# Performance work log

Measured on AMD Instinct MI355X. Metric: run time of the kernel, lower is better.

## Reference

```python
import jax, jax.numpy as jnp
import numpy as np

HEADS = 16


def fenwick_mask(T):
    # Boolean [T, T] mask: diagonal + Fenwick-tree lookback positions, causal.
    m = np.zeros((T, T), dtype=bool)
    for i in range(T):
        j = i + 1
        while j <= T:
            m[i, j - 1] = True
            j += j & -j
        step = 1
        while i - step >= 0:
            m[i, i - step] = True
            step *= 2
    m &= np.tril(np.ones((T, T), dtype=bool))  # causal
    return jnp.asarray(m)


def setup_inputs() -> dict:
    key = jax.random.key(0)
    ks = jax.random.split(key, 4)
    B, T, C = 2, 2048, 1024
    x = jax.random.normal(ks[0], (B, T, C), dtype=jnp.float32)
    W_qkv = jax.random.normal(ks[1], (C, 3 * C), dtype=jnp.float32) * (C ** -0.5)
    b_qkv = jnp.zeros((3 * C,), dtype=jnp.float32)
    W_proj = jax.random.normal(ks[2], (C, C), dtype=jnp.float32) * (C ** -0.5)
    b_proj = jnp.zeros((C,), dtype=jnp.float32)
    return {"x": x, "W_qkv": W_qkv, "b_qkv": b_qkv, "W_proj": W_proj, "b_proj": b_proj}


def reference(x, W_qkv, b_qkv, W_proj, b_proj):
    B, T, C = x.shape
    H = HEADS
    Dh = C // H
    scale = Dh ** -0.5
    qkv = (x @ W_qkv + b_qkv).reshape(B, T, 3, H, Dh)
    qkv = jnp.transpose(qkv, (2, 0, 3, 1, 4))  # [3, B, H, T, Dh]
    q, k, v = qkv[0], qkv[1], qkv[2]
    attn = jnp.einsum('bhtd,bhsd->bhts', q, k) * scale  # [B, H, T, T]
    mask = fenwick_mask(T)  # trace-time constant
    attn = jnp.where(mask[None, None], attn, -jnp.inf)
    attn = jax.nn.softmax(attn, axis=-1)
    out = jnp.einsum('bhts,bhsd->bhtd', attn, v)  # [B, H, T, Dh]
    out = jnp.transpose(out, (0, 2, 1, 3)).reshape(B, T, C)
    return out @ W_proj + b_proj
```

## Files before the change

kernel.cpp:

```cpp
#include <hip/hip_runtime.h>
#include <hip/hip_bf16.h>


typedef unsigned short ushort_t;
typedef __attribute__((ext_vector_type(8))) short s16x8;
typedef __attribute__((ext_vector_type(4))) float f32x4;

#define T_SEQ 2048
#define C_DIM 1024
#define HEADS 16

__device__ __forceinline__ ushort_t f2bf(float f) {
    union { float f; unsigned u; } v{f};
    unsigned r = v.u + 0x7FFFu + ((v.u >> 16) & 1u);
    return (ushort_t)(r >> 16);
}
__device__ __forceinline__ float bf2f(ushort_t u) {
    union { unsigned u; float f; } v{((unsigned)u) << 16};
    return v.f;
}

__device__ __forceinline__ void async16(const ushort_t* g, ushort_t* l) {
    __builtin_amdgcn_global_load_lds(
        (const __attribute__((address_space(1))) void*)g,
        (__attribute__((address_space(3))) void*)l, 16, 0, 0);
}

__global__ void cvt_bf16(const float* __restrict__ in, ushort_t* __restrict__ out, int n4) {
    int i = blockIdx.x * blockDim.x + threadIdx.x;
    if (i < n4) {
        float4 f = ((const float4*)in)[i];
        ushort4 o;
        o.x = f2bf(f.x); o.y = f2bf(f.y); o.z = f2bf(f.z); o.w = f2bf(f.w);
        ((ushort4*)out)[i] = o;
    }
}

__global__ void transpose_bf16(const float* __restrict__ W, ushort_t* __restrict__ WT,
                               int K, int N) {
    __shared__ ushort_t tile[32][33];
    int nb = blockIdx.x * 32, kb = blockIdx.y * 32;
    int tx = threadIdx.x, ty = threadIdx.y;
    #pragma unroll
    for (int i = ty; i < 32; i += 8)
        tile[i][tx] = f2bf(W[(size_t)(kb + i) * N + nb + tx]);
    __syncthreads();
    #pragma unroll
    for (int i = ty; i < 32; i += 8)
        WT[(size_t)(nb + i) * K + kb + tx] = tile[tx][i];
}

template <bool OUT_BF16>
__global__ void gemm_bt(const ushort_t* __restrict__ A, const ushort_t* __restrict__ BT,
                        const float* __restrict__ bias, void* __restrict__ C,
                        int N, int K) {
    __shared__ ushort_t lsA[128 * 64];
    __shared__ ushort_t lsB[128 * 64];

    const int tid  = threadIdx.x;
    const int wave = tid >> 6;
    const int lane = tid & 63;
    const int row0 = blockIdx.x * 128;
    const int col0 = blockIdx.y * 128;
    const int wr   = (wave >> 1) * 64;
    const int wc   = (wave & 1) * 64;
    const int lrow = lane & 15;
    const int quad = lane >> 4;
    const int crow = lane >> 3;
    const int ccol = (lane & 7) * 8;

    f32x4 acc[4][4] = {};

    for (int k0 = 0; k0 < K; k0 += 64) {
        #pragma unroll
        for (int it = 0; it < 4; ++it) {
            const int chunk = it * 4 + wave;
            const int r = chunk * 8 + crow;
            async16(A  + (size_t)(row0 + r) * K + (k0 + ccol), lsA + chunk * 512);
            async16(BT + (size_t)(col0 + r) * K + (k0 + ccol), lsB + chunk * 512);
        }
        __syncthreads();
        #pragma unroll
        for (int kk = 0; kk < 64; kk += 32) {
            s16x8 af[4], bfr[4];
            #pragma unroll
            for (int i = 0; i < 4; ++i)
                af[i] = *(const s16x8*)(lsA + (wr + i * 16 + lrow) * 64 + kk + quad * 8);
            #pragma unroll
            for (int j = 0; j < 4; ++j)
                bfr[j] = *(const s16x8*)(lsB + (wc + j * 16 + lrow) * 64 + kk + quad * 8);
            #pragma unroll
            for (int i = 0; i < 4; ++i)
                #pragma unroll
                for (int j = 0; j < 4; ++j)
                    acc[i][j] = __builtin_amdgcn_mfma_f32_16x16x32_bf16(
                        af[i], bfr[j], acc[i][j], 0, 0, 0);
        }
        __syncthreads();
    }

    #pragma unroll
    for (int i = 0; i < 4; ++i) {
        #pragma unroll
        for (int j = 0; j < 4; ++j) {
            const int col = col0 + wc + j * 16 + lrow;
            const float bv = bias[col];
            #pragma unroll
            for (int r = 0; r < 4; ++r) {
                const int row = row0 + wr + i * 16 + quad * 4 + r;
                const float v = acc[i][j][r] + bv;
                if (OUT_BF16)
                    ((ushort_t*)C)[(size_t)row * N + col] = f2bf(v);
                else
                    ((float*)C)[(size_t)row * N + col] = v;
            }
        }
    }
}

__global__ void fenwick_attn(const ushort_t* __restrict__ QKV, ushort_t* __restrict__ AO) {
    const int lane = threadIdx.x & 63;
    const int wid  = blockIdx.x * 4 + (threadIdx.x >> 6);
    const int tile = wid & 255;
    const int bh   = wid >> 8;
    const int h    = bh & (HEADS - 1);
    const int b    = bh >> 4;
    const int tl   = lane >> 3;
    const int g    = lane & 7;
    const int t    = tile * 8 + tl;

    const ushort_t* base = QKV + (size_t)(b * T_SEQ) * 3072 + h * 64 + g * 8;

    float qf[8];
    {
        s16x8 qv = *(const s16x8*)(base + (size_t)t * 3072);
        #pragma unroll
        for (int e = 0; e < 8; ++e) qf[e] = bf2f((ushort_t)qv[e]);
    }

    float logit[12];
    int   pos[12];
    float mx = -1e30f;
    #pragma unroll
    for (int s = 0; s < 12; ++s) {
        const int step = (s == 0) ? 0 : (1 << (s - 1));
        const bool act = (step <= t);
        const int p = act ? (t - step) : t;
        pos[s] = p;
        s16x8 kv = *(const s16x8*)(base + (size_t)p * 3072 + 1024);
        float l = 0.f;
        #pragma unroll
        for (int e = 0; e < 8; ++e) l = fmaf(qf[e], bf2f((ushort_t)kv[e]), l);
        l += __shfl_xor(l, 1, 64);
        l += __shfl_xor(l, 2, 64);
        l += __shfl_xor(l, 4, 64);
        l *= 0.125f;
        logit[s] = act ? l : -1e30f;
        mx = fmaxf(mx, logit[s]);
    }

    float denom = 0.f;
    float ov[8] = {};
    #pragma unroll
    for (int s = 0; s < 12; ++s) {
        const float w = __expf(logit[s] - mx);
        denom += w;
        s16x8 vv = *(const s16x8*)(base + (size_t)pos[s] * 3072 + 2048);
        #pragma unroll
        for (int e = 0; e < 8; ++e) ov[e] = fmaf(w, bf2f((ushort_t)vv[e]), ov[e]);
    }

    const float inv = 1.f / denom;
    s16x8 os;
    #pragma unroll
    for (int e = 0; e < 8; ++e) os[e] = (short)f2bf(ov[e] * inv);
    *(s16x8*)(AO + (size_t)(b * T_SEQ + t) * C_DIM + h * 64 + g * 8) = os;
}

extern "C" void kernel_launch(void* const* d_in, const int* in_sizes, int n_in,
                              void* d_out, int out_size, void* d_ws, size_t ws_size,
                              hipStream_t stream) {
    const float* x      = (const float*)d_in[0];
    const float* W_qkv  = (const float*)d_in[1];
    const float* b_qkv  = (const float*)d_in[2];
    const float* W_proj = (const float*)d_in[3];
    const float* b_proj = (const float*)d_in[4];
    float* out = (float*)d_out;

    char* ws = (char*)d_ws;
    ushort_t* xb     = (ushort_t*)(ws);
    ushort_t* WqkvT  = (ushort_t*)(ws + (size_t)8  * 1048576);
    ushort_t* QKVb   = (ushort_t*)(ws + (size_t)14 * 1048576);
    ushort_t* AO     = (ushort_t*)(ws + (size_t)38 * 1048576);
    ushort_t* WprojT = (ushort_t*)(ws + (size_t)46 * 1048576);

    cvt_bf16<<<4096, 256, 0, stream>>>(x, xb, 4096 * 1024 / 4);
    transpose_bf16<<<dim3(96, 32), dim3(32, 8), 0, stream>>>(W_qkv, WqkvT, 1024, 3072);
    transpose_bf16<<<dim3(32, 32), dim3(32, 8), 0, stream>>>(W_proj, WprojT, 1024, 1024);

    gemm_bt<true ><<<dim3(32, 24), 256, 0, stream>>>(xb, WqkvT, b_qkv, QKVb, 3072, 1024);
    fenwick_attn<<<2048, 256, 0, stream>>>(QKVb, AO);
    gemm_bt<false><<<dim3(32, 8), 256, 0, stream>>>(AO, WprojT, b_proj, out, 1024, 1024);
}
```

Baseline: 164.6 us.

## Fuse prep kernels, swizzle GEMM LDS layout, shrink projection GEMM tile

Merges the bf16 conversion of x and both weight transposes into one launch, which removes two kernel launches. Adds an XOR swizzle to the LDS tile layout in both GEMMs so the MFMA fragment reads avoid bank conflicts. The output projection GEMM gets its own kernel with a 128x64 tile, doubling its grid to 512 blocks for better CU occupancy on a small problem. In exchange the code is longer and each block does less reuse in the projection GEMM.

```diff
diff --git a/kernel.cpp b/kernel.cpp
--- a/kernel.cpp
+++ b/kernel.cpp
@@ -26,34 +26,41 @@
         (__attribute__((address_space(3))) void*)l, 16, 0, 0);
 }
 
-__global__ void cvt_bf16(const float* __restrict__ in, ushort_t* __restrict__ out, int n4) {
-    int i = blockIdx.x * blockDim.x + threadIdx.x;
-    if (i < n4) {
-        float4 f = ((const float4*)in)[i];
+__global__ void prep(const float* __restrict__ x, ushort_t* __restrict__ xb,
+                     const float* __restrict__ Wq, ushort_t* __restrict__ WqT,
+                     const float* __restrict__ Wp, ushort_t* __restrict__ WpT) {
+    const int bid = blockIdx.x;
+    const int tid = threadIdx.x;
+    if (bid < 4096) {
+        const int i = bid * 256 + tid;
+        float4 f = ((const float4*)x)[i];
         ushort4 o;
         o.x = f2bf(f.x); o.y = f2bf(f.y); o.z = f2bf(f.z); o.w = f2bf(f.w);
-        ((ushort4*)out)[i] = o;
-    }
-}
-
-__global__ void transpose_bf16(const float* __restrict__ W, ushort_t* __restrict__ WT,
-                               int K, int N) {
-    __shared__ ushort_t tile[32][33];
-    int nb = blockIdx.x * 32, kb = blockIdx.y * 32;
-    int tx = threadIdx.x, ty = threadIdx.y;
-    #pragma unroll
-    for (int i = ty; i < 32; i += 8)
-        tile[i][tx] = f2bf(W[(size_t)(kb + i) * N + nb + tx]);
-    __syncthreads();
-    #pragma unroll
-    for (int i = ty; i < 32; i += 8)
-        WT[(size_t)(nb + i) * K + kb + tx] = tile[tx][i];
-}
-
-template <bool OUT_BF16>
-__global__ void gemm_bt(const ushort_t* __restrict__ A, const ushort_t* __restrict__ BT,
-                        const float* __restrict__ bias, void* __restrict__ C,
-                        int N, int K) {
+        ((ushort4*)xb)[i] = o;
+    } else {
+        __shared__ ushort_t tile[32][33];
+        const float* W; ushort_t* WT; int N, nb, kb;
+        if (bid < 7168) {
+            const int tb = bid - 4096;
+            W = Wq; WT = WqT; N = 3072; nb = (tb % 96) * 32; kb = (tb / 96) * 32;
+        } else {
+            const int tb = bid - 7168;
+            W = Wp; WT = WpT; N = 1024; nb = (tb & 31) * 32; kb = (tb >> 5) * 32;
+        }
+        const int tx = tid & 31, ty = tid >> 5;
+        #pragma unroll
+        for (int i = ty; i < 32; i += 8)
+            tile[i][tx] = f2bf(W[(size_t)(kb + i) * N + nb + tx]);
+        __syncthreads();
+        #pragma unroll
+        for (int i = ty; i < 32; i += 8)
+            WT[(size_t)(nb + i) * 1024 + kb + tx] = tile[tx][i];
+    }
+}
+
+__global__ void gemm_qkv(const ushort_t* __restrict__ A, const ushort_t* __restrict__ BT,
+                         const float* __restrict__ bias, ushort_t* __restrict__ C,
+                         int N, int K) {
     __shared__ ushort_t lsA[128 * 64];
     __shared__ ushort_t lsB[128 * 64];
 
@@ -67,7 +74,8 @@
     const int lrow = lane & 15;
     const int quad = lane >> 4;
     const int crow = lane >> 3;
-    const int ccol = (lane & 7) * 8;
+    const int gcol = ((lane & 7) ^ crow) * 8;
+    const int d3   = lrow & 7;
 
     f32x4 acc[4][4] = {};
 
@@ -76,19 +84,21 @@
         for (int it = 0; it < 4; ++it) {
             const int chunk = it * 4 + wave;
             const int r = chunk * 8 + crow;
-            async16(A  + (size_t)(row0 + r) * K + (k0 + ccol), lsA + chunk * 512);
-            async16(BT + (size_t)(col0 + r) * K + (k0 + ccol), lsB + chunk * 512);
+            async16(A  + (size_t)(row0 + r) * K + (k0 + gcol), lsA + chunk * 512);
+            async16(BT + (size_t)(col0 + r) * K + (k0 + gcol), lsB + chunk * 512);
         }
         __syncthreads();
         #pragma unroll
         for (int kk = 0; kk < 64; kk += 32) {
+            const int g = (kk >> 3) + quad;
+            const int slot = (g ^ d3) << 3;
             s16x8 af[4], bfr[4];
             #pragma unroll
             for (int i = 0; i < 4; ++i)
-                af[i] = *(const s16x8*)(lsA + (wr + i * 16 + lrow) * 64 + kk + quad * 8);
+                af[i] = *(const s16x8*)(lsA + (wr + i * 16 + lrow) * 64 + slot);
             #pragma unroll
             for (int j = 0; j < 4; ++j)
-                bfr[j] = *(const s16x8*)(lsB + (wc + j * 16 + lrow) * 64 + kk + quad * 8);
+                bfr[j] = *(const s16x8*)(lsB + (wc + j * 16 + lrow) * 64 + slot);
             #pragma unroll
             for (int i = 0; i < 4; ++i)
                 #pragma unroll
@@ -108,11 +118,76 @@
             #pragma unroll
             for (int r = 0; r < 4; ++r) {
                 const int row = row0 + wr + i * 16 + quad * 4 + r;
-                const float v = acc[i][j][r] + bv;
-                if (OUT_BF16)
-                    ((ushort_t*)C)[(size_t)row * N + col] = f2bf(v);
-                else
-                    ((float*)C)[(size_t)row * N + col] = v;
+                C[(size_t)row * N + col] = f2bf(acc[i][j][r] + bv);
+            }
+        }
+    }
+}
+
+__global__ void gemm_proj(const ushort_t* __restrict__ A, const ushort_t* __restrict__ BT,
+                          const float* __restrict__ bias, float* __restrict__ C,
+                          int N, int K) {
+    __shared__ ushort_t lsA[128 * 64];
+    __shared__ ushort_t lsB[64 * 64];
+
+    const int tid  = threadIdx.x;
+    const int wave = tid >> 6;
+    const int lane = tid & 63;
+    const int row0 = blockIdx.x * 128;
+    const int col0 = blockIdx.y * 64;
+    const int lrow = lane & 15;
+    const int quad = lane >> 4;
+    const int crow = lane >> 3;
+    const int gcol = ((lane & 7) ^ crow) * 8;
+    const int d3   = lrow & 7;
+
+    f32x4 acc[2][4] = {};
+
+    for (int k0 = 0; k0 < K; k0 += 64) {
+        #pragma unroll
+        for (int it = 0; it < 4; ++it) {
+            const int chunk = it * 4 + wave;
+            const int r = chunk * 8 + crow;
+            async16(A + (size_t)(row0 + r) * K + (k0 + gcol), lsA + chunk * 512);
+        }
+        #pragma unroll
+        for (int it = 0; it < 2; ++it) {
+            const int chunk = it * 4 + wave;
+            const int r = chunk * 8 + crow;
+            async16(BT + (size_t)(col0 + r) * K + (k0 + gcol), lsB + chunk * 512);
+        }
+        __syncthreads();
+        #pragma unroll
+        for (int kk = 0; kk < 64; kk += 32) {
+            const int g = (kk >> 3) + quad;
+            const int slot = (g ^ d3) << 3;
+            s16x8 af[2], bfr[4];
+            #pragma unroll
+            for (int i = 0; i < 2; ++i)
+                af[i] = *(const s16x8*)(lsA + (wave * 32 + i * 16 + lrow) * 64 + slot);
+            #pragma unroll
+            for (int j = 0; j < 4; ++j)
+                bfr[j] = *(const s16x8*)(lsB + (j * 16 + lrow) * 64 + slot);
+            #pragma unroll
+            for (int i = 0; i < 2; ++i)
+                #pragma unroll
+                for (int j = 0; j < 4; ++j)
+                    acc[i][j] = __builtin_amdgcn_mfma_f32_16x16x32_bf16(
+                        af[i], bfr[j], acc[i][j], 0, 0, 0);
+        }
+        __syncthreads();
+    }
+
+    #pragma unroll
+    for (int i = 0; i < 2; ++i) {
+        #pragma unroll
+        for (int j = 0; j < 4; ++j) {
+            const int col = col0 + j * 16 + lrow;
+            const float bv = bias[col];
+            #pragma unroll
+            for (int r = 0; r < 4; ++r) {
+                const int row = row0 + wave * 32 + i * 16 + quad * 4 + r;
+                C[(size_t)row * N + col] = acc[i][j][r] + bv;
             }
         }
     }
@@ -194,11 +269,8 @@
     ushort_t* AO     = (ushort_t*)(ws + (size_t)38 * 1048576);
     ushort_t* WprojT = (ushort_t*)(ws + (size_t)46 * 1048576);
 
-    cvt_bf16<<<4096, 256, 0, stream>>>(x, xb, 4096 * 1024 / 4);
-    transpose_bf16<<<dim3(96, 32), dim3(32, 8), 0, stream>>>(W_qkv, WqkvT, 1024, 3072);
-    transpose_bf16<<<dim3(32, 32), dim3(32, 8), 0, stream>>>(W_proj, WprojT, 1024, 1024);
-
-    gemm_bt<true ><<<dim3(32, 24), 256, 0, stream>>>(xb, WqkvT, b_qkv, QKVb, 3072, 1024);
+    prep<<<8192, 256, 0, stream>>>(x, xb, W_qkv, WqkvT, W_proj, WprojT);
+    gemm_qkv<<<dim3(32, 24), 256, 0, stream>>>(xb, WqkvT, b_qkv, QKVb, 3072, 1024);
     fenwick_attn<<<2048, 256, 0, stream>>>(QKVb, AO);
-    gemm_bt<false><<<dim3(32, 8), 256, 0, stream>>>(AO, WprojT, b_proj, out, 1024, 1024);
-}
+    gemm_proj<<<dim3(32, 16), 256, 0, stream>>>(AO, WprojT, b_proj, out, 1024, 1024);
+}
```

Result: faster. 145.5 us (-11.6%).
